# Kernel optimization log

Measured on AMD Instinct MI355X. Metric: run time of the kernel, lower is better.

## Reference

```python
import jax, jax.numpy as jnp
import numpy as np
from math import sqrt

B, L, H, E = 4, 2048, 16, 64
S, D = 2048, 64

def setup_inputs() -> dict:
    key = jax.random.key(0)
    kq, kk, kv = jax.random.split(key, 3)
    queries = jax.random.normal(kq, (B, L, H, E), dtype=jnp.float32)
    keys = jax.random.normal(kk, (B, S, H, E), dtype=jnp.float32)
    values = jax.random.normal(kv, (B, S, H, D), dtype=jnp.float32)
    return {"queries": queries, "keys": keys, "values": values}

def reference(queries, keys, values):
    Bq, Lq, Hq, Eq = queries.shape
    Sk = keys.shape[1]
    scale = 1.0 / sqrt(Eq)
    # scores: [B, H, L, S]
    scores = jnp.einsum('blhe,bshe->bhls', queries, keys)
    # TriangularCausalMask: mask positions where key index > query index
    causal = jnp.triu(jnp.ones((Lq, Sk), dtype=bool), k=1)  # True above diagonal
    scores = jnp.where(causal, -jnp.inf, scores)
    A = jax.nn.softmax(scale * scores, axis=-1)  # dropout p=0.0 -> identity
    V = jnp.einsum('bhls,bshd->blhd', A, values)
    return V
```

## Files before the change

kernel.cpp:

```cpp
#include <hip/hip_runtime.h>
#include <hip/hip_bf16.h>

typedef __attribute__((ext_vector_type(8))) short short8;
typedef __attribute__((ext_vector_type(4))) short short4v;
typedef __attribute__((ext_vector_type(16))) float f32x16;

constexpr int Bc = 4;
constexpr int Lc = 2048;
constexpr int Sc = 2048;
constexpr int Hc = 16;
constexpr int Ec = 64;
constexpr int Dc = 64;
constexpr int QBLK = 128;
constexpr int KBLK = 64;
constexpr int NQT  = Lc / QBLK;

__device__ __forceinline__ unsigned short b16(float x) {
  __bf16 h = (__bf16)x;
  return __builtin_bit_cast(unsigned short, h);
}
__device__ __forceinline__ unsigned pk2(float lo, float hi) {
  return (unsigned)b16(lo) | ((unsigned)b16(hi) << 16);
}
__device__ __forceinline__ short8 cvt8(float4 a, float4 b) {
  short8 w;
  w[0] = (short)b16(a.x); w[1] = (short)b16(a.y);
  w[2] = (short)b16(a.z); w[3] = (short)b16(a.w);
  w[4] = (short)b16(b.x); w[5] = (short)b16(b.y);
  w[6] = (short)b16(b.z); w[7] = (short)b16(b.w);
  return w;
}
__device__ __forceinline__ short8 mk8(unsigned d0, unsigned d1, unsigned d2, unsigned d3) {
  union { unsigned u[4]; short8 s; } t;
  t.u[0] = d0; t.u[1] = d1; t.u[2] = d2; t.u[3] = d3;
  return t.s;
}

struct KV { float4 k[4]; float4 v[4]; };

__global__ __launch_bounds__(256, 2)
void fattn_kernel(const float* __restrict__ Qg, const float* __restrict__ Kg,
                  const float* __restrict__ Vg, float* __restrict__ Og) {
  __shared__ unsigned short Kl[2][KBLK * 64];
  __shared__ unsigned short Vl[2][KBLK * 64];

  const int tid  = (int)threadIdx.x;
  const int wave = tid >> 6;
  const int lane = tid & 63;
  const int q32  = lane & 31;
  const int hi   = lane >> 5;

  const int pb = (int)blockIdx.x;
  const int bh = (int)blockIdx.y;
  const int b  = bh >> 4;
  const int h  = bh & 15;

  const int qA   = pb;
  const int qB   = NQT - 1 - pb;
  const int q0A  = qA * QBLK + wave * 32;
  const int q0B  = qB * QBLK + wave * 32;
  const int nchA = 2 * pb + 2;
  const int nchB = 2 * qB + 2;

  const float QSCALE = 0.125f * 1.44269504088896341f;
  auto loadQ = [&](int q0, short8 (&qf)[4]) {
    const float* qp = Qg + (((size_t)(b * Lc + q0 + q32)) * Hc + h) * Ec;
#pragma unroll
    for (int c = 0; c < 4; ++c) {
      const float4* p4 = (const float4*)(qp + c * 16 + hi * 8);
      float4 x = p4[0], y = p4[1];
      x.x *= QSCALE; x.y *= QSCALE; x.z *= QSCALE; x.w *= QSCALE;
      y.x *= QSCALE; y.y *= QSCALE; y.z *= QSCALE; y.w *= QSCALE;
      qf[c] = cvt8(x, y);
    }
  };
  short8 qfA[4], qfB[4];
  loadQ(q0A, qfA);
  loadQ(q0B, qfB);

  short8 ones;
#pragma unroll
  for (int j = 0; j < 8; ++j) ones[j] = (short)0x3F80;

  const int s  = tid >> 2;
  const int e0 = (tid & 3) << 4;

  auto loadKV = [&](int ch) {
    KV r;
    const size_t row = (((size_t)(b * Sc + ch * KBLK + s)) * Hc + h);
    const float4* kp4 = (const float4*)(Kg + row * Ec + e0);
    const float4* vp4 = (const float4*)(Vg + row * Dc + e0);
#pragma unroll
    for (int i = 0; i < 4; ++i) { r.k[i] = kp4[i]; r.v[i] = vp4[i]; }
    return r;
  };

  auto writeKV = [&](const KV& r, int buf) {
    short8 w0 = cvt8(r.k[0], r.k[1]);
    short8 w1 = cvt8(r.k[2], r.k[3]);
    const int c0 = e0 >> 3;
    *(short8*)&Kl[buf][s * 64 + (((c0    ) ^ (s & 7)) << 3)] = w0;
    *(short8*)&Kl[buf][s * 64 + (((c0 + 1) ^ (s & 7)) << 3)] = w1;
    short8 wv0 = cvt8(r.v[0], r.v[1]);
    short8 wv1 = cvt8(r.v[2], r.v[3]);
    const int vt = ((s >> 2) * 4 + (tid & 3)) * 64 + (s & 3) * 16;
    *(short8*)&Vl[buf][vt]     = wv0;
    *(short8*)&Vl[buf][vt + 8] = wv1;
  };

  f32x16 accoA0 = (f32x16)(0.f), accoA1 = (f32x16)(0.f), acclA = (f32x16)(0.f);
  f32x16 accoB0 = (f32x16)(0.f), accoB1 = (f32x16)(0.f), acclB = (f32x16)(0.f);
  float mA = -1e30f, mB = -1e30f;

  auto doTile = [&](int ch, int cur, int q0w, const short8 (&qf)[4],
                    f32x16& acco0, f32x16& acco1, f32x16& accl, float& m_run) {
    const int s0 = ch * 64;
    const bool act0 = (s0 <= q0w);
    if (!act0) return;
    const bool act1  = (s0 + 32 <= q0w);
    const bool diag0 = (s0 == q0w);
    const bool diag1 = (s0 + 32 == q0w);

    auto qk = [&](int sb) {
      f32x16 acc = (f32x16)(0.f);
      const int sr = sb * 32 + q32;
      const int rb = sr * 64;
      const int sw = sr & 7;
#pragma unroll
      for (int c = 0; c < 4; ++c) {
        short8 kf = *(const short8*)&Kl[cur][rb + (((2 * c + hi) ^ sw) << 3)];
        acc = __builtin_amdgcn_mfma_f32_32x32x16_bf16(kf, qf[c], acc, 0, 0, 0);
      }
      return acc;
    };
    f32x16 S0 = qk(0);
    f32x16 S1;
    if (act1) S1 = qk(1);

    const int tq = q32 - 4 * hi;
    if (diag0) {
#pragma unroll
      for (int r = 0; r < 16; ++r)
        if (((r & 3) + 8 * (r >> 2)) > tq) S0[r] = -1e30f;
    }
    if (act1 && diag1) {
#pragma unroll
      for (int r = 0; r < 16; ++r)
        if (((r & 3) + 8 * (r >> 2)) > tq) S1[r] = -1e30f;
    }

    float pmax = S0[0];
#pragma unroll
    for (int r = 1; r < 16; ++r) pmax = fmaxf(pmax, S0[r]);
    if (act1) {
#pragma unroll
      for (int r = 0; r < 16; ++r) pmax = fmaxf(pmax, S1[r]);
    }
    {
      unsigned px = __builtin_bit_cast(unsigned, pmax);
      auto sw = __builtin_amdgcn_permlane32_swap(px, px, false, false);
      pmax = fmaxf(__builtin_bit_cast(float, (unsigned)sw[0]),
                   __builtin_bit_cast(float, (unsigned)sw[1]));
    }

    if (!__all(pmax - m_run <= 8.0f)) {
      const float mnew  = fmaxf(m_run, pmax);
      const float alpha = exp2f(m_run - mnew);
      m_run = mnew;
      const int hib = hi << 4;
      const int av  = __builtin_bit_cast(int, alpha);
#pragma unroll
      for (int r = 0; r < 16; ++r) {
        const int addr = hib + 4 * ((r & 3) + 8 * (r >> 2));
        float ar = __builtin_bit_cast(float, __builtin_amdgcn_ds_bpermute(addr, av));
        acco0[r] *= ar; acco1[r] *= ar; accl[r] *= ar;
      }
    }

#pragma unroll
    for (int r = 0; r < 16; ++r) S0[r] = exp2f(S0[r] - m_run);
    if (act1) {
#pragma unroll
      for (int r = 0; r < 16; ++r) S1[r] = exp2f(S1[r] - m_run);
    }

    auto mkpa = [&](const f32x16& P, int a, int bidx) {
      unsigned A0 = pk2(P[4 * a + 0],    P[4 * a + 1]);
      unsigned A1 = pk2(P[4 * a + 2],    P[4 * a + 3]);
      unsigned B0 = pk2(P[4 * bidx + 0], P[4 * bidx + 1]);
      unsigned B1 = pk2(P[4 * bidx + 2], P[4 * bidx + 3]);
      auto r0 = __builtin_amdgcn_permlane32_swap(A0, B0, false, false);
      auto r1 = __builtin_amdgcn_permlane32_swap(A1, B1, false, false);
      return mk8((unsigned)r0[0], (unsigned)r1[0], (unsigned)r0[1], (unsigned)r1[1]);
    };
    short8 pa0 = mkpa(S0, 0, 1);
    short8 pa1 = mkpa(S0, 2, 3);
    short8 pa2, pa3;
    if (act1) { pa2 = mkpa(S1, 0, 1); pa3 = mkpa(S1, 2, 3); }

    const unsigned vbase = (unsigned)(size_t)(&Vl[cur][0]);
    const unsigned vcol  = ((unsigned)(q32 & 15) << 3);
    short4v vlo[2][4], vhi[2][4];
#pragma unroll
    for (int ks = 0; ks < 4; ++ks) {
      if (ks < 2 || act1) {
#pragma unroll
        for (int dt = 0; dt < 2; ++dt) {
          const unsigned a0 = vbase +
            ((((unsigned)(4 * ks + 2 * hi) * 4u) + 2u * dt + (unsigned)(q32 >> 4)) << 7) + vcol;
          asm volatile("ds_read_b64_tr_b16 %0, %1 offset:0"   : "=&v"(vlo[dt][ks]) : "v"(a0));
          asm volatile("ds_read_b64_tr_b16 %0, %1 offset:512" : "=&v"(vhi[dt][ks]) : "v"(a0));
        }
      }
    }

    accl = __builtin_amdgcn_mfma_f32_32x32x16_bf16(pa0, ones, accl, 0, 0, 0);
    accl = __builtin_amdgcn_mfma_f32_32x32x16_bf16(pa1, ones, accl, 0, 0, 0);
    if (act1) {
      accl = __builtin_amdgcn_mfma_f32_32x32x16_bf16(pa2, ones, accl, 0, 0, 0);
      accl = __builtin_amdgcn_mfma_f32_32x32x16_bf16(pa3, ones, accl, 0, 0, 0);
    }

    asm volatile("s_waitcnt lgkmcnt(0)" ::: "memory");
    __builtin_amdgcn_sched_barrier(0);

#pragma unroll
    for (int dt = 0; dt < 2; ++dt) {
      f32x16& ac = dt ? acco1 : acco0;
      short8 vf0 = __builtin_shufflevector(vlo[dt][0], vhi[dt][0], 0,1,2,3,4,5,6,7);
      short8 vf1 = __builtin_shufflevector(vlo[dt][1], vhi[dt][1], 0,1,2,3,4,5,6,7);
      ac = __builtin_amdgcn_mfma_f32_32x32x16_bf16(pa0, vf0, ac, 0, 0, 0);
      ac = __builtin_amdgcn_mfma_f32_32x32x16_bf16(pa1, vf1, ac, 0, 0, 0);
      if (act1) {
        short8 vf2 = __builtin_shufflevector(vlo[dt][2], vhi[dt][2], 0,1,2,3,4,5,6,7);
        short8 vf3 = __builtin_shufflevector(vlo[dt][3], vhi[dt][3], 0,1,2,3,4,5,6,7);
        ac = __builtin_amdgcn_mfma_f32_32x32x16_bf16(pa2, vf2, ac, 0, 0, 0);
        ac = __builtin_amdgcn_mfma_f32_32x32x16_bf16(pa3, vf3, ac, 0, 0, 0);
      }
    }
  };

  { KV r0 = loadKV(0); writeKV(r0, 0); }
  __syncthreads();

  int cur = 0;
  for (int ch = 0; ch < nchB; ++ch) {
    const bool pref = (ch + 1 < nchB);
    KV nxt;
    if (pref) nxt = loadKV(ch + 1);

    doTile(ch, cur, q0B, qfB, accoB0, accoB1, acclB, mB);
    if (ch < nchA) doTile(ch, cur, q0A, qfA, accoA0, accoA1, acclA, mA);

    if (pref) writeKV(nxt, cur ^ 1);
    __syncthreads();
    cur ^= 1;
  }

  auto epi = [&](int q0w, const f32x16& acco0, const f32x16& acco1, const f32x16& accl) {
#pragma unroll
    for (int r = 0; r < 16; ++r) {
      const int q_loc = (r & 3) + 8 * (r >> 2) + 4 * hi;
      const int q = q0w + q_loc;
      const float inv = 1.0f / accl[r];
      float* op = Og + (((size_t)(b * Lc + q)) * Hc + h) * Dc + q32;
      op[0]  = acco0[r] * inv;
      op[32] = acco1[r] * inv;
    }
  };
  epi(q0A, accoA0, accoA1, acclA);
  epi(q0B, accoB0, accoB1, acclB);
}

extern "C" void kernel_launch(void* const* d_in, const int* in_sizes, int n_in,
                              void* d_out, int out_size, void* d_ws, size_t ws_size,
                              hipStream_t stream) {
  const float* Q = (const float*)d_in[0];
  const float* K = (const float*)d_in[1];
  const float* V = (const float*)d_in[2];
  float* O = (float*)d_out;
  dim3 grid(NQT / 2, Bc * Hc);
  fattn_kernel<<<grid, 256, 0, stream>>>(Q, K, V, O);
}
```

Baseline: 111.9 us.

## Split KV loop across two blocks and merge partial outputs

Adds a split-K (flash-decoding style) mode: each (q-tile pair, bh) is processed by two blocks, each handling alternating KV chunks, writing bf16 partial outputs plus running max and sum to workspace. A second merge kernel combines the partials with rescaled weights. This doubles the grid (8x64x2 blocks) to raise occupancy and parallelism on the many-CU GPU. The cost is an extra launch, workspace traffic and bf16 rounding of the unnormalized partial outputs. Interleaving chunks means each block still loads every other tile, which keeps the causal work balanced between the two halves.

```diff
diff --git a/kernel.cpp b/kernel.cpp
--- a/kernel.cpp
+++ b/kernel.cpp
@@ -14,6 +14,9 @@
 constexpr int QBLK = 128;
 constexpr int KBLK = 64;
 constexpr int NQT  = Lc / QBLK;
+constexpr int NROWS = Bc * Lc * Hc;
+constexpr size_t OPART_ELEMS = (size_t)Bc * Lc * Hc * Dc;
+constexpr size_t WS_NEED = 2 * OPART_ELEMS * 2  + 2 * (size_t)NROWS * 8 ;
 
 __device__ __forceinline__ unsigned short b16(float x) {
   __bf16 h = (__bf16)x;
@@ -21,6 +24,10 @@
 }
 __device__ __forceinline__ unsigned pk2(float lo, float hi) {
   return (unsigned)b16(lo) | ((unsigned)b16(hi) << 16);
+}
+__device__ __forceinline__ float bf2f(unsigned short u) {
+  unsigned v = (unsigned)u << 16;
+  return __builtin_bit_cast(float, v);
 }
 __device__ __forceinline__ short8 cvt8(float4 a, float4 b) {
   short8 w;
@@ -38,9 +45,11 @@
 
 struct KV { float4 k[4]; float4 v[4]; };
 
+template <int SPLIT>
 __global__ __launch_bounds__(256, 2)
 void fattn_kernel(const float* __restrict__ Qg, const float* __restrict__ Kg,
-                  const float* __restrict__ Vg, float* __restrict__ Og) {
+                  const float* __restrict__ Vg, float* __restrict__ Og,
+                  unsigned short* __restrict__ OPart, float2* __restrict__ Stats) {
   __shared__ unsigned short Kl[2][KBLK * 64];
   __shared__ unsigned short Vl[2][KBLK * 64];
 
@@ -50,8 +59,9 @@
   const int q32  = lane & 31;
   const int hi   = lane >> 5;
 
-  const int pb = (int)blockIdx.x;
-  const int bh = (int)blockIdx.y;
+  const int pb   = (int)blockIdx.x;
+  const int bh   = (int)blockIdx.y;
+  const int half = (SPLIT == 2) ? (int)blockIdx.z : 0;
   const int b  = bh >> 4;
   const int h  = bh & 15;
 
@@ -240,14 +250,14 @@
     }
   };
 
-  { KV r0 = loadKV(0); writeKV(r0, 0); }
+  { KV r0 = loadKV(half); writeKV(r0, 0); }
   __syncthreads();
 
   int cur = 0;
-  for (int ch = 0; ch < nchB; ++ch) {
-    const bool pref = (ch + 1 < nchB);
+  for (int ch = half; ch < nchB; ch += SPLIT) {
+    const bool pref = (ch + SPLIT < nchB);
     KV nxt;
-    if (pref) nxt = loadKV(ch + 1);
+    if (pref) nxt = loadKV(ch + SPLIT);
 
     doTile(ch, cur, q0B, qfB, accoB0, accoB1, acclB, mB);
     if (ch < nchA) doTile(ch, cur, q0A, qfA, accoA0, accoA1, acclA, mA);
@@ -257,19 +267,55 @@
     cur ^= 1;
   }
 
-  auto epi = [&](int q0w, const f32x16& acco0, const f32x16& acco1, const f32x16& accl) {
+  auto epi = [&](int q0w, const f32x16& acco0, const f32x16& acco1,
+                 const f32x16& accl, float m_run) {
 #pragma unroll
     for (int r = 0; r < 16; ++r) {
       const int q_loc = (r & 3) + 8 * (r >> 2) + 4 * hi;
       const int q = q0w + q_loc;
-      const float inv = 1.0f / accl[r];
-      float* op = Og + (((size_t)(b * Lc + q)) * Hc + h) * Dc + q32;
-      op[0]  = acco0[r] * inv;
-      op[32] = acco1[r] * inv;
-    }
-  };
-  epi(q0A, accoA0, accoA1, acclA);
-  epi(q0B, accoB0, accoB1, acclB);
+      const size_t rowbase = (((size_t)(b * Lc + q)) * Hc + h) * Dc;
+      if constexpr (SPLIT == 1) {
+        const float inv = 1.0f / accl[r];
+        Og[rowbase + q32]      = acco0[r] * inv;
+        Og[rowbase + q32 + 32] = acco1[r] * inv;
+      } else {
+        unsigned short* op = OPart + (size_t)half * OPART_ELEMS + rowbase;
+        op[q32]      = b16(acco0[r]);
+        op[q32 + 32] = b16(acco1[r]);
+        const float mr = __builtin_bit_cast(float,
+            __builtin_amdgcn_ds_bpermute(4 * q_loc, __builtin_bit_cast(int, m_run)));
+        if (q32 == 0) {
+          float2 st; st.x = mr; st.y = accl[r];
+          Stats[(size_t)half * NROWS + (size_t)(b * Lc + q) * Hc + h] = st;
+        }
+      }
+    }
+  };
+  epi(q0A, accoA0, accoA1, acclA, mA);
+  epi(q0B, accoB0, accoB1, acclB, mB);
+}
+
+__global__ __launch_bounds__(256)
+void merge_kernel(const unsigned short* __restrict__ OPart,
+                  const float2* __restrict__ Stats, float* __restrict__ Og) {
+  const int gid = (int)(blockIdx.x * 256 + threadIdx.x);
+  const int row = gid >> 4;
+  const int d0  = (gid & 15) << 2;
+  if (row >= NROWS) return;
+  float2 s0 = Stats[row];
+  float2 s1 = Stats[(size_t)NROWS + row];
+  const float M  = fmaxf(s0.x, s1.x);
+  const float w0 = exp2f(s0.x - M);
+  const float w1 = exp2f(s1.x - M);
+  const float inv = 1.0f / (s0.y * w0 + s1.y * w1);
+  const ushort4 a = *(const ushort4*)(OPart + (size_t)row * 64 + d0);
+  const ushort4 c = *(const ushort4*)(OPart + OPART_ELEMS + (size_t)row * 64 + d0);
+  float4 o;
+  o.x = (bf2f(a.x) * w0 + bf2f(c.x) * w1) * inv;
+  o.y = (bf2f(a.y) * w0 + bf2f(c.y) * w1) * inv;
+  o.z = (bf2f(a.z) * w0 + bf2f(c.z) * w1) * inv;
+  o.w = (bf2f(a.w) * w0 + bf2f(c.w) * w1) * inv;
+  *(float4*)(Og + (size_t)row * 64 + d0) = o;
 }
 
 extern "C" void kernel_launch(void* const* d_in, const int* in_sizes, int n_in,
@@ -279,6 +325,16 @@
   const float* K = (const float*)d_in[1];
   const float* V = (const float*)d_in[2];
   float* O = (float*)d_out;
-  dim3 grid(NQT / 2, Bc * Hc);
-  fattn_kernel<<<grid, 256, 0, stream>>>(Q, K, V, O);
-}
+  unsigned short* opart = (unsigned short*)d_ws;
+  float2* stats = (float2*)((char*)d_ws + 2 * OPART_ELEMS * 2);
+
+  if (ws_size >= WS_NEED) {
+    dim3 grid(NQT / 2, Bc * Hc, 2);
+    fattn_kernel<2><<<grid, 256, 0, stream>>>(Q, K, V, O, opart, stats);
+    const int nthr = NROWS * 16;
+    merge_kernel<<<(nthr + 255) / 256, 256, 0, stream>>>(opart, stats, O);
+  } else {
+    dim3 grid(NQT / 2, Bc * Hc, 1);
+    fattn_kernel<1><<<grid, 256, 0, stream>>>(Q, K, V, O, opart, stats);
+  }
+}
```

Measured after the change: 131.5 us. 1.18x slower.
